# Optimization experiments

Hardware: AMD Instinct MI355X
Metric: run time of the kernel (lower is better)

## Reference

```python
import jax, jax.numpy as jnp
import numpy as np

MULT = 32       # multiplicity per irrep type (both input and output)
N = 262144      # number of nodes/examples
LS = (0, 1, 2, 3)  # irrep degrees -> block sizes 2l+1 = 1,3,5,7


def setup_inputs() -> dict:
    key = jax.random.key(0)
    keys = jax.random.split(key, 2 * len(LS))
    inp = {}
    for j, l in enumerate(LS):
        m = 2 * l + 1
        inp[f"x{l}"] = jax.random.normal(keys[2 * j], (N, MULT, m), dtype=jnp.float32)
        inp[f"W{l}"] = jax.random.normal(keys[2 * j + 1], (MULT, MULT, m), dtype=jnp.float32)
    return inp


def reference(x0, x1, x2, x3, W0, W1, W2, W3):
    # Block-diagonal equivariant linear: for each irrep type l,
    # out[n, o, m] = sum_i W_l[o, i, m] * x_l[n, i, m]
    # (elementwise in m within each 2l+1 block, summed over input multiplicity i).
    outs = [
        jnp.einsum("nim,oim->nom", x, W)
        for x, W in ((x0, W0), (x1, W1), (x2, W2), (x3, W3))
    ]
    # Concatenate flattened irrep blocks -> [N, MULT*(1+3+5+7)] = [N, 512]
    return jnp.concatenate([o.reshape(o.shape[0], -1) for o in outs], axis=-1)
```

## Files before the change

kernel.cpp:

```cpp
#include <hip/hip_runtime.h>
#include <hip/hip_fp16.h>


#define NTH 512
#define TN  32

typedef _Float16 f16x8 __attribute__((ext_vector_type(8)));
typedef float    f32x4 __attribute__((ext_vector_type(4)));

#define LGKM0_BAR() do { asm volatile("s_waitcnt lgkmcnt(0)" ::: "memory"); \
                         __builtin_amdgcn_s_barrier(); } while (0)

template<int M_, int PB>
__device__ __forceinline__ void stageW(const float* __restrict__ src,
                                       __half* __restrict__ dst, int tid)
{
    #pragma unroll
    for (int it = 0; it < (256 * M_ + NTH - 1) / NTH; ++it) {
        const int f = tid + it * NTH;
        if (f < 256 * M_) {
            float4 v = ((const float4*)src)[f];
            const float vf[4] = {v.x, v.y, v.z, v.w};
            const int e0 = 4 * f;
            #pragma unroll
            for (int k = 0; k < 4; ++k) {
                const int e = e0 + k;
                const int o = e / (32 * M_);
                const int r = e - o * (32 * M_);
                const int i = r / M_, mi = r - i * M_;
                const int p = PB + mi;
                dst[p * 1280 + o * 40 + ((i + 8 * p) & 31)] = __float2half(vf[k]);
            }
        }
    }
}

template<int M_, int PB>
__device__ __forceinline__ void mkoff(int tloc, int* offk)
{
    const int e0    = 4 * tloc;
    const int nodel = e0 / (32 * M_);
    const int r0    = e0 - nodel * (32 * M_);
    #pragma unroll
    for (int k = 0; k < 4; ++k) {
        const int ii = (r0 + k) / M_, mi = (r0 + k) - ii * M_;
        const int p  = PB + mi;
        offk[k] = p * 1280 + nodel * 40 + ((ii + 8 * p) & 31);
    }
}

__device__ __forceinline__ void plane_info(int p, int& Mm, int& BASE, int& MI)
{
    if (p == 0)     { Mm = 1; BASE = 0;   MI = 0;     }
    else if (p < 4) { Mm = 3; BASE = 32;  MI = p - 1; }
    else if (p < 9) { Mm = 5; BASE = 128; MI = p - 4; }
    else            { Mm = 7; BASE = 288; MI = p - 9; }
}

__device__ __forceinline__ void store_tile(const __half* __restrict__ OC,
                                           float* __restrict__ dst, int tid)
{
    #pragma unroll
    for (int it = 0; it < 4; ++it) {
        const int d0   = 8 * tid + 4096 * it;
        const int node = d0 >> 9, col = d0 & 511;
        uint4 h8 = *(const uint4*)(OC + node * 520 + col);
        const __half2* hp = (const __half2*)&h8;
        float2 f0 = __half22float2(hp[0]);
        float2 f1 = __half22float2(hp[1]);
        float2 f2 = __half22float2(hp[2]);
        float2 f3 = __half22float2(hp[3]);
        *(float4*)(dst + d0)     = make_float4(f0.x, f0.y, f1.x, f1.y);
        *(float4*)(dst + d0 + 4) = make_float4(f2.x, f2.y, f3.x, f3.y);
    }
}

__global__ __launch_bounds__(NTH, 4) void eqlin(
    const float* __restrict__ x0, const float* __restrict__ x1,
    const float* __restrict__ x2, const float* __restrict__ x3,
    const float* __restrict__ w0, const float* __restrict__ w1,
    const float* __restrict__ w2, const float* __restrict__ w3,
    float* __restrict__ out, int n_tiles)
{
    __shared__ __align__(16) __half XT[20480];
    __shared__ __align__(16) __half OC[16640];
    const int tid  = threadIdx.x;
    const int wave = tid >> 6;
    const int lane = tid & 63;

    int thrg, Mg, offk[4];
    const float* xb;
    bool isM1 = false;
    if (tid < 32)       { thrg = 32;  Mg = 1; xb = x0; mkoff<1, 0>(tid,       offk); isM1 = true; }
    else if (tid < 128) { thrg = 96;  Mg = 3; xb = x1; mkoff<3, 1>(tid - 32,  offk); }
    else if (tid < 288) { thrg = 160; Mg = 5; xb = x2; mkoff<5, 4>(tid - 128, offk); }
    else                { thrg = 224; Mg = 7; xb = x3; mkoff<7, 9>(tid - 288, offk); }
    const int  tloc    = (tid < 32) ? tid : (tid < 128) ? tid - 32 : (tid < 288) ? tid - 128 : tid - 288;
    const long jstride = 4L * thrg;
    const long tstride = (long)gridDim.x * 1024L * Mg;

    const float* srcp = xb + (long)blockIdx.x * (1024L * Mg) + 4 * tloc;
    float4 pf[8];
    #pragma unroll
    for (int j = 0; j < 8; ++j)
        pf[j] = *(const float4*)(srcp + j * jstride);

    stageW<1, 0>(w0, XT, tid);
    stageW<3, 1>(w1, XT, tid);
    stageW<5, 4>(w2, XT, tid);
    stageW<7, 9>(w3, XT, tid);

    const int lrow = lane & 15;
    const int lk8  = (lane >> 4) * 8;
    const int crow = (lane >> 4) * 4;
    const int p0   = wave * 2, p1 = wave * 2 + 1;
    const int c0   = (lk8 + 8 * p0) & 31;
    const int c1   = (lk8 + 8 * p1) & 31;

    LGKM0_BAR();
    f16x8 Wf[2][2];
    Wf[0][0] = *(const f16x8*)(XT + p0 * 1280 + lrow * 40 + c0);
    Wf[0][1] = *(const f16x8*)(XT + p0 * 1280 + (lrow + 16) * 40 + c0);
    Wf[1][0] = *(const f16x8*)(XT + p1 * 1280 + lrow * 40 + c1);
    Wf[1][1] = *(const f16x8*)(XT + p1 * 1280 + (lrow + 16) * 40 + c1);
    LGKM0_BAR();

    int Mm0, BASE0, MI0, Mm1, BASE1, MI1;
    plane_info(p0, Mm0, BASE0, MI0);
    plane_info(p1, Mm1, BASE1, MI1);

    long prev_node0 = -1;
    for (int t = blockIdx.x; t < n_tiles; t += gridDim.x) {
        const long node0 = (long)t * TN;

        #pragma unroll
        for (int j = 0; j < 8; ++j) {
            const float4 v = pf[j];
            const int jb = j * 160;
            if (isM1) {
                __half2* p = (__half2*)&XT[offk[0] + jb];
                p[0] = __floats2half2_rn(v.x, v.y);
                p[1] = __floats2half2_rn(v.z, v.w);
            } else {
                XT[offk[0] + jb] = __float2half(v.x);
                XT[offk[1] + jb] = __float2half(v.y);
                XT[offk[2] + jb] = __float2half(v.z);
                XT[offk[3] + jb] = __float2half(v.w);
            }
        }
        if (t + (long)gridDim.x < n_tiles) {
            srcp += tstride;
            #pragma unroll
            for (int j = 0; j < 8; ++j)
                pf[j] = *(const float4*)(srcp + j * jstride);
        }
        if (prev_node0 >= 0)
            store_tile(OC, out + prev_node0 * 512, tid);

        LGKM0_BAR();

        f32x4 acc[2][2][2] = {};
        {
            const __half* xp0 = XT + p0 * 1280 + lrow * 40 + c0;
            const __half* xp1 = XT + p1 * 1280 + lrow * 40 + c1;
            f16x8 A00 = *(const f16x8*)xp0;
            f16x8 A01 = *(const f16x8*)(xp0 + 640);
            f16x8 A10 = *(const f16x8*)xp1;
            f16x8 A11 = *(const f16x8*)(xp1 + 640);
            acc[0][0][0] = __builtin_amdgcn_mfma_f32_16x16x32_f16(A00, Wf[0][0], acc[0][0][0], 0, 0, 0);
            acc[0][0][1] = __builtin_amdgcn_mfma_f32_16x16x32_f16(A00, Wf[0][1], acc[0][0][1], 0, 0, 0);
            acc[0][1][0] = __builtin_amdgcn_mfma_f32_16x16x32_f16(A01, Wf[0][0], acc[0][1][0], 0, 0, 0);
            acc[0][1][1] = __builtin_amdgcn_mfma_f32_16x16x32_f16(A01, Wf[0][1], acc[0][1][1], 0, 0, 0);
            acc[1][0][0] = __builtin_amdgcn_mfma_f32_16x16x32_f16(A10, Wf[1][0], acc[1][0][0], 0, 0, 0);
            acc[1][0][1] = __builtin_amdgcn_mfma_f32_16x16x32_f16(A10, Wf[1][1], acc[1][0][1], 0, 0, 0);
            acc[1][1][0] = __builtin_amdgcn_mfma_f32_16x16x32_f16(A11, Wf[1][0], acc[1][1][0], 0, 0, 0);
            acc[1][1][1] = __builtin_amdgcn_mfma_f32_16x16x32_f16(A11, Wf[1][1], acc[1][1][1], 0, 0, 0);
        }
        #pragma unroll
        for (int pl = 0; pl < 2; ++pl) {
            const int Mm   = pl ? Mm1   : Mm0;
            const int BASE = pl ? BASE1 : BASE0;
            const int MI   = pl ? MI1   : MI0;
            #pragma unroll
            for (int nh = 0; nh < 2; ++nh)
            #pragma unroll
            for (int oh = 0; oh < 2; ++oh) {
                const int o     = oh * 16 + lrow;
                const int colb  = BASE + o * Mm + MI;
                const int nodeb = nh * 16 + crow;
                #pragma unroll
                for (int r = 0; r < 4; ++r)
                    OC[(nodeb + r) * 520 + colb] = __float2half(acc[pl][nh][oh][r]);
            }
        }

        LGKM0_BAR();
        prev_node0 = node0;
    }

    if (prev_node0 >= 0)
        store_tile(OC, out + prev_node0 * 512, tid);
}

extern "C" void kernel_launch(void* const* d_in, const int* in_sizes, int n_in,
                              void* d_out, int out_size, void* d_ws, size_t ws_size,
                              hipStream_t stream)
{
    long tot = 0;
    for (int i = 0; i < n_in; ++i) tot += in_sizes[i];
    const long N = (tot - 16384) / 512;
    const int  ms[4] = {1, 3, 5, 7};
    const float* xs[4]  = {nullptr, nullptr, nullptr, nullptr};
    const float* wsp[4] = {nullptr, nullptr, nullptr, nullptr};
    for (int i = 0; i < n_in; ++i) {
        const long s = in_sizes[i];
        for (int l = 0; l < 4; ++l) {
            if (s == N * 32 * ms[l])      xs[l]  = (const float*)d_in[i];
            else if (s == 1024L * ms[l])  wsp[l] = (const float*)d_in[i];
        }
    }
    const int n_tiles = (int)(N / TN);
    const int grid = 512;
    hipLaunchKernelGGL(eqlin, dim3(grid), dim3(NTH), 0, stream,
                       xs[0], xs[1], xs[2], xs[3],
                       wsp[0], wsp[1], wsp[2], wsp[3],
                       (float*)d_out, n_tiles);
}
```

Baseline: 210.0 us.

## Halve node tile and double-buffer LDS into three-stage software pipeline

Result: no change. 207.4 us (median of 2 runs) (-1.2%).

```diff
diff --git a/kernel.cpp b/kernel.cpp
--- a/kernel.cpp
+++ b/kernel.cpp
@@ -3,7 +3,7 @@
 
 
 #define NTH 512
-#define TN  32
+#define TN  16
 
 typedef _Float16 f16x8 __attribute__((ext_vector_type(8)));
 typedef float    f32x4 __attribute__((ext_vector_type(4)));
@@ -45,7 +45,7 @@
     for (int k = 0; k < 4; ++k) {
         const int ii = (r0 + k) / M_, mi = (r0 + k) - ii * M_;
         const int p  = PB + mi;
-        offk[k] = p * 1280 + nodel * 40 + ((ii + 8 * p) & 31);
+        offk[k] = p * 640 + nodel * 40 + ((ii + 8 * p) & 31);
     }
 }
 
@@ -57,14 +57,14 @@
     else            { Mm = 7; BASE = 288; MI = p - 9; }
 }
 
-__device__ __forceinline__ void store_tile(const __half* __restrict__ OC,
+__device__ __forceinline__ void store_tile(const __half* __restrict__ OCb,
                                            float* __restrict__ dst, int tid)
 {
     #pragma unroll
-    for (int it = 0; it < 4; ++it) {
+    for (int it = 0; it < 2; ++it) {
         const int d0   = 8 * tid + 4096 * it;
         const int node = d0 >> 9, col = d0 & 511;
-        uint4 h8 = *(const uint4*)(OC + node * 520 + col);
+        uint4 h8 = *(const uint4*)(OCb + node * 520 + col);
         const __half2* hp = (const __half2*)&h8;
         float2 f0 = __half22float2(hp[0]);
         float2 f1 = __half22float2(hp[1]);
@@ -82,8 +82,8 @@
     const float* __restrict__ w2, const float* __restrict__ w3,
     float* __restrict__ out, int n_tiles)
 {
-    __shared__ __align__(16) __half XT[20480];
-    __shared__ __align__(16) __half OC[16640];
+    __shared__ __align__(16) __half XT[2][10240];
+    __shared__ __align__(16) __half OC[2][8320];
     const int tid  = threadIdx.x;
     const int wave = tid >> 6;
     const int lane = tid & 63;
@@ -97,109 +97,105 @@
     else                { thrg = 224; Mg = 7; xb = x3; mkoff<7, 9>(tid - 288, offk); }
     const int  tloc    = (tid < 32) ? tid : (tid < 128) ? tid - 32 : (tid < 288) ? tid - 128 : tid - 288;
     const long jstride = 4L * thrg;
-    const long tstride = (long)gridDim.x * 1024L * Mg;
-
-    const float* srcp = xb + (long)blockIdx.x * (1024L * Mg) + 4 * tloc;
-    float4 pf[8];
-    #pragma unroll
-    for (int j = 0; j < 8; ++j)
+    const long tstride = (long)gridDim.x * 512L * Mg;
+
+    const float* srcp = xb + (long)blockIdx.x * (512L * Mg) + 4 * tloc;
+    float4 pf[4];
+    #pragma unroll
+    for (int j = 0; j < 4; ++j)
         pf[j] = *(const float4*)(srcp + j * jstride);
-
-    stageW<1, 0>(w0, XT, tid);
-    stageW<3, 1>(w1, XT, tid);
-    stageW<5, 4>(w2, XT, tid);
-    stageW<7, 9>(w3, XT, tid);
 
     const int lrow = lane & 15;
     const int lk8  = (lane >> 4) * 8;
     const int crow = (lane >> 4) * 4;
-    const int p0   = wave * 2, p1 = wave * 2 + 1;
+    const int p0   = wave * 2, p1 = p0 + 1;
     const int c0   = (lk8 + 8 * p0) & 31;
     const int c1   = (lk8 + 8 * p1) & 31;
 
+    __half* WS = &XT[0][0];
+    stageW<1, 0>(w0, WS, tid);
+    stageW<3, 1>(w1, WS, tid);
+    stageW<5, 4>(w2, WS, tid);
+    stageW<7, 9>(w3, WS, tid);
     LGKM0_BAR();
     f16x8 Wf[2][2];
-    Wf[0][0] = *(const f16x8*)(XT + p0 * 1280 + lrow * 40 + c0);
-    Wf[0][1] = *(const f16x8*)(XT + p0 * 1280 + (lrow + 16) * 40 + c0);
-    Wf[1][0] = *(const f16x8*)(XT + p1 * 1280 + lrow * 40 + c1);
-    Wf[1][1] = *(const f16x8*)(XT + p1 * 1280 + (lrow + 16) * 40 + c1);
+    Wf[0][0] = *(const f16x8*)(WS + p0 * 1280 + lrow * 40 + c0);
+    Wf[0][1] = *(const f16x8*)(WS + p0 * 1280 + (lrow + 16) * 40 + c0);
+    Wf[1][0] = *(const f16x8*)(WS + p1 * 1280 + lrow * 40 + c1);
+    Wf[1][1] = *(const f16x8*)(WS + p1 * 1280 + (lrow + 16) * 40 + c1);
     LGKM0_BAR();
 
     int Mm0, BASE0, MI0, Mm1, BASE1, MI1;
     plane_info(p0, Mm0, BASE0, MI0);
     plane_info(p1, Mm1, BASE1, MI1);
 
-    long prev_node0 = -1;
-    for (int t = blockIdx.x; t < n_tiles; t += gridDim.x) {
-        const long node0 = (long)t * TN;
-
-        #pragma unroll
-        for (int j = 0; j < 8; ++j) {
-            const float4 v = pf[j];
-            const int jb = j * 160;
-            if (isM1) {
-                __half2* p = (__half2*)&XT[offk[0] + jb];
-                p[0] = __floats2half2_rn(v.x, v.y);
-                p[1] = __floats2half2_rn(v.z, v.w);
-            } else {
-                XT[offk[0] + jb] = __float2half(v.x);
-                XT[offk[1] + jb] = __float2half(v.y);
-                XT[offk[2] + jb] = __float2half(v.z);
-                XT[offk[3] + jb] = __float2half(v.w);
-            }
-        }
-        if (t + (long)gridDim.x < n_tiles) {
-            srcp += tstride;
+    const long gstep = gridDim.x;
+    for (long k = 0;; ++k) {
+        const long ts  = (long)blockIdx.x + k * gstep;
+        const long tst = ts - 2 * gstep;
+        const bool do_stage = ts < n_tiles;
+        const bool do_mfma  = (k >= 1) && (ts - gstep) < n_tiles;
+        const bool do_store = (k >= 2) && tst < n_tiles;
+        if (!do_stage && !do_mfma && !do_store) break;
+        const int A = (int)(k & 1), B = A ^ 1;
+
+        if (do_stage) {
+            __half* XA = &XT[A][0];
             #pragma unroll
-            for (int j = 0; j < 8; ++j)
-                pf[j] = *(const float4*)(srcp + j * jstride);
-        }
-        if (prev_node0 >= 0)
-            store_tile(OC, out + prev_node0 * 512, tid);
+            for (int j = 0; j < 4; ++j) {
+                const float4 v = pf[j];
+                const int jb = j * 160;
+                if (isM1) {
+                    __half2* p = (__half2*)&XA[offk[0] + jb];
+                    p[0] = __floats2half2_rn(v.x, v.y);
+                    p[1] = __floats2half2_rn(v.z, v.w);
+                } else {
+                    XA[offk[0] + jb] = __float2half(v.x);
+                    XA[offk[1] + jb] = __float2half(v.y);
+                    XA[offk[2] + jb] = __float2half(v.z);
+                    XA[offk[3] + jb] = __float2half(v.w);
+                }
+            }
+            if (ts + gstep < n_tiles) {
+                srcp += tstride;
+                #pragma unroll
+                for (int j = 0; j < 4; ++j)
+                    pf[j] = *(const float4*)(srcp + j * jstride);
+            }
+        }
+
+        if (do_store)
+            store_tile(&OC[B][0], out + tst * (TN * 512L), tid);
+
+        if (do_mfma) {
+            const __half* XB = &XT[B][0];
+            f32x4 acc[2][2] = {};
+            f16x8 A0 = *(const f16x8*)(XB + p0 * 640 + lrow * 40 + c0);
+            f16x8 A1 = *(const f16x8*)(XB + p1 * 640 + lrow * 40 + c1);
+            acc[0][0] = __builtin_amdgcn_mfma_f32_16x16x32_f16(A0, Wf[0][0], acc[0][0], 0, 0, 0);
+            acc[0][1] = __builtin_amdgcn_mfma_f32_16x16x32_f16(A0, Wf[0][1], acc[0][1], 0, 0, 0);
+            acc[1][0] = __builtin_amdgcn_mfma_f32_16x16x32_f16(A1, Wf[1][0], acc[1][0], 0, 0, 0);
+            acc[1][1] = __builtin_amdgcn_mfma_f32_16x16x32_f16(A1, Wf[1][1], acc[1][1], 0, 0, 0);
+
+            __half* OA = &OC[A][0];
+            #pragma unroll
+            for (int pl = 0; pl < 2; ++pl) {
+                const int Mm   = pl ? Mm1   : Mm0;
+                const int BASE = pl ? BASE1 : BASE0;
+                const int MI   = pl ? MI1   : MI0;
+                #pragma unroll
+                for (int oh = 0; oh < 2; ++oh) {
+                    const int o    = oh * 16 + lrow;
+                    const int colb = BASE + o * Mm + MI;
+                    #pragma unroll
+                    for (int r = 0; r < 4; ++r)
+                        OA[(crow + r) * 520 + colb] = __float2half(acc[pl][oh][r]);
+                }
+            }
+        }
 
         LGKM0_BAR();
-
-        f32x4 acc[2][2][2] = {};
-        {
-            const __half* xp0 = XT + p0 * 1280 + lrow * 40 + c0;
-            const __half* xp1 = XT + p1 * 1280 + lrow * 40 + c1;
-            f16x8 A00 = *(const f16x8*)xp0;
-            f16x8 A01 = *(const f16x8*)(xp0 + 640);
-            f16x8 A10 = *(const f16x8*)xp1;
-            f16x8 A11 = *(const f16x8*)(xp1 + 640);
-            acc[0][0][0] = __builtin_amdgcn_mfma_f32_16x16x32_f16(A00, Wf[0][0], acc[0][0][0], 0, 0, 0);
-            acc[0][0][1] = __builtin_amdgcn_mfma_f32_16x16x32_f16(A00, Wf[0][1], acc[0][0][1], 0, 0, 0);
-            acc[0][1][0] = __builtin_amdgcn_mfma_f32_16x16x32_f16(A01, Wf[0][0], acc[0][1][0], 0, 0, 0);
-            acc[0][1][1] = __builtin_amdgcn_mfma_f32_16x16x32_f16(A01, Wf[0][1], acc[0][1][1], 0, 0, 0);
-            acc[1][0][0] = __builtin_amdgcn_mfma_f32_16x16x32_f16(A10, Wf[1][0], acc[1][0][0], 0, 0, 0);
-            acc[1][0][1] = __builtin_amdgcn_mfma_f32_16x16x32_f16(A10, Wf[1][1], acc[1][0][1], 0, 0, 0);
-            acc[1][1][0] = __builtin_amdgcn_mfma_f32_16x16x32_f16(A11, Wf[1][0], acc[1][1][0], 0, 0, 0);
-            acc[1][1][1] = __builtin_amdgcn_mfma_f32_16x16x32_f16(A11, Wf[1][1], acc[1][1][1], 0, 0, 0);
-        }
-        #pragma unroll
-        for (int pl = 0; pl < 2; ++pl) {
-            const int Mm   = pl ? Mm1   : Mm0;
-            const int BASE = pl ? BASE1 : BASE0;
-            const int MI   = pl ? MI1   : MI0;
-            #pragma unroll
-            for (int nh = 0; nh < 2; ++nh)
-            #pragma unroll
-            for (int oh = 0; oh < 2; ++oh) {
-                const int o     = oh * 16 + lrow;
-                const int colb  = BASE + o * Mm + MI;
-                const int nodeb = nh * 16 + crow;
-                #pragma unroll
-                for (int r = 0; r < 4; ++r)
-                    OC[(nodeb + r) * 520 + colb] = __float2half(acc[pl][nh][oh][r]);
-            }
-        }
-
-        LGKM0_BAR();
-        prev_node0 = node0;
-    }
-
-    if (prev_node0 >= 0)
-        store_tile(OC, out + prev_node0 * 512, tid);
+    }
 }
 
 extern "C" void kernel_launch(void* const* d_in, const int* in_sizes, int n_in,
```
